# Kernel tuning notes

Hardware: AMD Instinct MI355X
Metric: run time of the kernel (lower is better)

The kernel has to match this reference:

```python
import jax, jax.numpy as jnp
import numpy as np

N_NODES = 100000
N_EDGES = 1200000
D = 64
GCN_LAYERS = 2
KEEP_PROB = 0.7


def setup_inputs() -> dict:
    key = jax.random.key(0)
    k1, k2, k3, k4, k5, k6, k7 = jax.random.split(key, 7)
    all_emb = jax.random.normal(k1, (N_NODES, D), dtype=jnp.float32)
    W = jax.random.normal(k2, (D, D), dtype=jnp.float32) * 0.05
    b = jax.random.normal(k3, (D,), dtype=jnp.float32) * 0.05
    # sparse adjacency values (e.g. normalized weights)
    vals = jax.random.uniform(k4, (N_EDGES,), dtype=jnp.float32)
    # per-layer dropout uniforms, mirrors torch.rand(len(values)) each layer
    drop_u = jax.random.uniform(k5, (GCN_LAYERS, N_EDGES), dtype=jnp.float32)
    rows = jax.random.randint(k6, (N_EDGES,), 0, N_NODES)
    cols = jax.random.randint(k7, (N_EDGES,), 0, N_NODES)
    return {"all_emb": all_emb, "W": W, "b": b, "vals": vals,
            "drop_u": drop_u, "rows": rows, "cols": cols}


def reference(all_emb, W, b, vals, drop_u, rows, cols):
    # emb[0] = fc(all_emb)
    acc = all_emb @ W.T + b  # [N, D]
    x = all_emb
    for layer in range(GCN_LAYERS):
        # edge dropout: keep iff (u + keep_prob) floors to 1, scale by 1/keep_prob
        keep = (drop_u[layer] + KEEP_PROB) >= 1.0
        v = jnp.where(keep, vals / KEEP_PROB, 0.0)  # [E]
        # SpMM: x <- A_dropped @ x via gather + segment-sum scatter
        msgs = v[:, None] * x[cols]  # [E, D]
        x = jax.ops.segment_sum(msgs, rows, num_segments=N_NODES)  # [N, D]
        acc = acc + x
    # mean over stacked (gcn_layers + 1) embeddings
    return acc / float(GCN_LAYERS + 1)
```

## Files before the change

kernel.cpp:

```cpp
#include <hip/hip_runtime.h>

#define N_NODES 100000
#define N_EDGES 1200000
#define D 64
#define KEEP_PROB 0.7f
#define INV_KEEP (1.0f / KEEP_PROB)
#define NBUCK 1564
#define MAXB 1024
#define PPART 256
#define CHUNK4 1172

#define ALOAD_I(p)   __hip_atomic_load((p), __ATOMIC_RELAXED, __HIP_MEMORY_SCOPE_AGENT)
#define ALOAD_U64(p) __hip_atomic_load((p), __ATOMIC_RELAXED, __HIP_MEMORY_SCOPE_AGENT)

__global__ __launch_bounds__(256) void zero_kernel(float4* __restrict__ p, int n4) {
    int i = blockIdx.x * 256 + threadIdx.x;
    if (i < n4) p[i] = make_float4(0.f, 0.f, 0.f, 0.f);
}
__global__ __launch_bounds__(256) void zero_ints_kernel(int* __restrict__ p, int n) {
    int i = blockIdx.x * 256 + threadIdx.x;
    if (i < n) p[i] = 0;
}

__global__ __launch_bounds__(256) void bucket_hist_kernel(const int4* __restrict__ rows4,
                                                          int* __restrict__ bcnt,
                                                          int* __restrict__ h) {
    __shared__ int hh[NBUCK];
    int p = blockIdx.x;
    int t = threadIdx.x;
    for (int i = t; i < NBUCK; i += 256) hh[i] = 0;
    __syncthreads();
    int i0 = p * CHUNK4;
    int i1 = i0 + CHUNK4;
    if (i1 > N_EDGES / 4) i1 = N_EDGES / 4;
    for (int i = i0 + t; i < i1; i += 256) {
        int4 r = rows4[i];
        atomicAdd(&hh[r.x >> 6], 1);
        atomicAdd(&hh[r.y >> 6], 1);
        atomicAdd(&hh[r.z >> 6], 1);
        atomicAdd(&hh[r.w >> 6], 1);
    }
    __syncthreads();
    int* hp = h + p * NBUCK;
    for (int i = t; i < NBUCK; i += 256) {
        int c = hh[i];
        hp[i] = c;
        if (c) atomicAdd(&bcnt[i << 4], c);
    }
}

__global__ __launch_bounds__(256) void bucket_scan_kernel(const int* __restrict__ bcnt,
                                                          int* __restrict__ bbase,
                                                          int* __restrict__ Pstart) {
    __shared__ int part[256];
    const int CH = 7;
    int t = threadIdx.x;
    int e[CH]; int s = 0;
    #pragma unroll
    for (int k = 0; k < CH; ++k) {
        int j = t * CH + k;
        e[k] = (j < NBUCK) ? ALOAD_I(&bcnt[j << 4]) : 0;
        s += e[k];
    }
    part[t] = s;
    __syncthreads();
    for (int d = 1; d < 256; d <<= 1) {
        int w = (t >= d) ? part[t - d] : 0;
        __syncthreads();
        part[t] += w;
        __syncthreads();
    }
    int run = part[t] - s;
    #pragma unroll
    for (int k = 0; k < CH; ++k) {
        int j = t * CH + k;
        if (j < NBUCK) { bbase[j] = run; run += e[k]; }
    }
    if (t == 255) bbase[NBUCK] = run;
    if (t == 0)   Pstart[N_NODES] = N_EDGES;
}

__global__ __launch_bounds__(256) void rebase_kernel(int* __restrict__ h,
                                                     const int* __restrict__ bbase) {
    int b = blockIdx.x * 256 + threadIdx.x;
    if (b >= NBUCK) return;
    int run = bbase[b];
    for (int p = 0; p < PPART; ++p) {
        int idx = p * NBUCK + b;
        int c = h[idx];
        h[idx] = run;
        run += c;
    }
}

__global__ __launch_bounds__(256) void partition_kernel(
    const int4*   __restrict__ rows4,
    const int4*   __restrict__ cols4,
    const float4* __restrict__ vals4,
    const float4* __restrict__ u04,
    const float4* __restrict__ u14,
    const int*    __restrict__ h,
    uint4*        __restrict__ edata) {
    __shared__ int cur[NBUCK];
    int p = blockIdx.x;
    int t = threadIdx.x;
    const int* hp = h + p * NBUCK;
    for (int i = t; i < NBUCK; i += 256) cur[i] = hp[i];
    __syncthreads();

    int i0 = p * CHUNK4;
    int i1 = i0 + CHUNK4;
    if (i1 > N_EDGES / 4) i1 = N_EDGES / 4;
    for (int i = i0 + t; i < i1; i += 256) {
        int4   r  = rows4[i];
        int4   c  = cols4[i];
        float4 v  = vals4[i];
        float4 u0 = u04[i];
        float4 u1 = u14[i];

        int p0 = atomicAdd(&cur[r.x >> 6], 1);
        int p1 = atomicAdd(&cur[r.y >> 6], 1);
        int p2 = atomicAdd(&cur[r.z >> 6], 1);
        int p3 = atomicAdd(&cur[r.w >> 6], 1);

        uint4 rec; float vv;
        vv = v.x * INV_KEEP;
        rec.x = (unsigned)c.x;
        rec.y = __float_as_uint((u0.x + KEEP_PROB >= 1.0f) ? vv : 0.f);
        rec.z = __float_as_uint((u1.x + KEEP_PROB >= 1.0f) ? vv : 0.f);
        rec.w = (unsigned)r.x;
        edata[p0] = rec;
        vv = v.y * INV_KEEP;
        rec.x = (unsigned)c.y;
        rec.y = __float_as_uint((u0.y + KEEP_PROB >= 1.0f) ? vv : 0.f);
        rec.z = __float_as_uint((u1.y + KEEP_PROB >= 1.0f) ? vv : 0.f);
        rec.w = (unsigned)r.y;
        edata[p1] = rec;
        vv = v.z * INV_KEEP;
        rec.x = (unsigned)c.z;
        rec.y = __float_as_uint((u0.z + KEEP_PROB >= 1.0f) ? vv : 0.f);
        rec.z = __float_as_uint((u1.z + KEEP_PROB >= 1.0f) ? vv : 0.f);
        rec.w = (unsigned)r.z;
        edata[p2] = rec;
        vv = v.w * INV_KEEP;
        rec.x = (unsigned)c.w;
        rec.y = __float_as_uint((u0.w + KEEP_PROB >= 1.0f) ? vv : 0.f);
        rec.z = __float_as_uint((u1.w + KEEP_PROB >= 1.0f) ? vv : 0.f);
        rec.w = (unsigned)r.w;
        edata[p3] = rec;
    }
}

__global__ __launch_bounds__(256) void finalize_kernel(
    uint4* __restrict__ edata,
    const int* __restrict__ bbase,
    int*   __restrict__ Pstart,
    uint4* __restrict__ scratch) {
    __shared__ uint4 recs[MAXB];
    __shared__ int cnt[64], cur[64], part[64];
    int b = blockIdx.x;
    int t = threadIdx.x;
    int base = bbase[b];
    int size = bbase[b + 1] - base;
    int row0 = b << 6;
    bool small = (size <= MAXB);

    const unsigned long long* src = (const unsigned long long*)(edata + base);
    if (small) {
        for (int i = t; i < size; i += 256) {
            unsigned long long lo = ALOAD_U64(src + 2 * i);
            unsigned long long hi = ALOAD_U64(src + 2 * i + 1);
            uint4 r;
            r.x = (unsigned)lo; r.y = (unsigned)(lo >> 32);
            r.z = (unsigned)hi; r.w = (unsigned)(hi >> 32);
            recs[i] = r;
        }
    } else {
        unsigned long long* dst = (unsigned long long*)(scratch + base);
        for (int i = t; i < 2 * size; i += 256) dst[i] = ALOAD_U64(src + i);
    }
    if (t < 64) cnt[t] = 0;
    __syncthreads();

    const uint4* gsrc = scratch + base;
    for (int i = t; i < size; i += 256) {
        unsigned rw = small ? recs[i].w : gsrc[i].w;
        atomicAdd(&cnt[rw & 63], 1);
    }
    __syncthreads();

    int v = (t < 64) ? cnt[t] : 0;
    if (t < 64) part[t] = v;
    __syncthreads();
    for (int d = 1; d < 64; d <<= 1) {
        int w = (t >= d && t < 64) ? part[t - d] : 0;
        __syncthreads();
        if (t < 64) part[t] += w;
        __syncthreads();
    }
    int R = N_NODES - row0; if (R > 64) R = 64;
    if (t < 64) {
        int pref = part[t] - v;
        cur[t] = pref;
        if (t < R) Pstart[row0 + t] = base + pref;
    }
    __syncthreads();

    for (int i = t; i < size; i += 256) {
        uint4 r = small ? recs[i] : gsrc[i];
        int lr = (int)(r.w & 63);
        int slot = atomicAdd(&cur[lr], 1);
        uint4 outrec;
        outrec.x = r.x; outrec.y = r.y;
        outrec.z = r.x; outrec.w = r.z;
        edata[base + slot] = outrec;
    }
}

__global__ __launch_bounds__(256) void spmm_gather_kernel(
    const float4* __restrict__ x_in,
    const unsigned long long* __restrict__ edata,
    const int*   __restrict__ Pstart,
    float4*      __restrict__ io,
    int layer) {
    int tid = blockIdx.x * 256 + threadIdx.x;
    int row = tid >> 4;
    int l16 = threadIdx.x & 15;
    if (row >= N_NODES) return;
    int start = ALOAD_I(&Pstart[row]);
    int end   = ALOAD_I(&Pstart[row + 1]);
    float4 acc = make_float4(0.f, 0.f, 0.f, 0.f);
    #pragma unroll 8
    for (int i = start; i < end; ++i) {
        unsigned long long rec = ALOAD_U64(&edata[2 * i + layer]);
        int   c = (int)(rec & 0xffffffffu);
        float v = __uint_as_float((unsigned)(rec >> 32));
        int  cc = (v != 0.f) ? c : 0;
        float4 x = x_in[(cc << 4) + l16];
        acc.x = fmaf(v, x.x, acc.x);
        acc.y = fmaf(v, x.y, acc.y);
        acc.z = fmaf(v, x.z, acc.z);
        acc.w = fmaf(v, x.w, acc.w);
    }
    int o = (row << 4) + l16;
    if (layer == 0) {
        io[o] = acc;
    } else {
        float4 p = io[o];
        p.x = (p.x + acc.x) * (1.0f / 3.0f);
        p.y = (p.y + acc.y) * (1.0f / 3.0f);
        p.z = (p.z + acc.z) * (1.0f / 3.0f);
        p.w = (p.w + acc.w) * (1.0f / 3.0f);
        io[o] = p;
    }
}

#define FMA4(A, E, WV) \
    A.x = fmaf(E, WV.x, A.x); A.y = fmaf(E, WV.y, A.y); \
    A.z = fmaf(E, WV.z, A.z); A.w = fmaf(E, WV.w, A.w);

__global__ __launch_bounds__(256, 4) void fc_add_kernel(
    const float* __restrict__ emb,
    const float* __restrict__ W,
    const float* __restrict__ b,
    const float* __restrict__ x1,
    float*       __restrict__ out) {
    __shared__ float Wt[D * 68];
    __shared__ float Es[64 * 68];

    int t = threadIdx.x;
    int n0 = blockIdx.x * 64;

    #pragma unroll
    for (int i = 0; i < 16; ++i) {
        int idx = i * 256 + t;
        Wt[(idx & 63) * 68 + (idx >> 6)] = W[idx];
    }
    #pragma unroll
    for (int i = 0; i < 4; ++i) {
        int idx4 = i * 256 + t;
        int n = idx4 >> 4;
        int k0 = (idx4 & 15) * 4;
        float4 v = make_float4(0.f, 0.f, 0.f, 0.f);
        if (n0 + n < N_NODES) v = *(const float4*)&emb[(n0 + n) * D + k0];
        *(float4*)&Es[n * 68 + k0] = v;
    }
    __syncthreads();

    int tj = t & 15;
    int tn = t >> 4;
    int j0 = tj * 4;

    float4 bb = *(const float4*)&b[j0];
    float4 acc[4];
    #pragma unroll
    for (int i = 0; i < 4; ++i) acc[i] = bb;

    const float* es = &Es[(tn * 4) * 68];
    #pragma unroll 4
    for (int kc = 0; kc < 16; ++kc) {
        int k = kc * 4;
        float4 w0 = *(const float4*)&Wt[(k + 0) * 68 + j0];
        float4 w1 = *(const float4*)&Wt[(k + 1) * 68 + j0];
        float4 w2 = *(const float4*)&Wt[(k + 2) * 68 + j0];
        float4 w3 = *(const float4*)&Wt[(k + 3) * 68 + j0];
        float4 e0 = *(const float4*)&es[0 * 68 + k];
        float4 e1 = *(const float4*)&es[1 * 68 + k];
        float4 e2 = *(const float4*)&es[2 * 68 + k];
        float4 e3 = *(const float4*)&es[3 * 68 + k];
        FMA4(acc[0], e0.x, w0); FMA4(acc[0], e0.y, w1);
        FMA4(acc[0], e0.z, w2); FMA4(acc[0], e0.w, w3);
        FMA4(acc[1], e1.x, w0); FMA4(acc[1], e1.y, w1);
        FMA4(acc[1], e1.z, w2); FMA4(acc[1], e1.w, w3);
        FMA4(acc[2], e2.x, w0); FMA4(acc[2], e2.y, w1);
        FMA4(acc[2], e2.z, w2); FMA4(acc[2], e2.w, w3);
        FMA4(acc[3], e3.x, w0); FMA4(acc[3], e3.y, w1);
        FMA4(acc[3], e3.z, w2); FMA4(acc[3], e3.w, w3);
    }

    #pragma unroll
    for (int i = 0; i < 4; ++i) {
        int n = n0 + tn * 4 + i;
        if (n < N_NODES) {
            float4 p = *(const float4*)&x1[n * D + j0];
            float4 a = acc[i];
            a.x += p.x; a.y += p.y; a.z += p.z; a.w += p.w;
            *(float4*)&out[n * D + j0] = a;
        }
    }
}

__global__ __launch_bounds__(256) void spmm_atomic_kernel(
    const float* __restrict__ x_in,
    const float* __restrict__ vals,
    const float* __restrict__ drop_u,
    const int*   __restrict__ rows,
    const int*   __restrict__ cols,
    float*       __restrict__ x_out) {
    int wave = (blockIdx.x * 256 + threadIdx.x) >> 6;
    int lane = threadIdx.x & 63;
    if (wave >= N_EDGES) return;
    float u = drop_u[wave];
    if (u + KEEP_PROB < 1.0f) return;
    float v = vals[wave] * INV_KEEP;
    atomicAdd(&x_out[rows[wave] * D + lane], v * x_in[cols[wave] * D + lane]);
}

__global__ __launch_bounds__(256) void scale_kernel(float4* __restrict__ p, int n4) {
    int i = blockIdx.x * 256 + threadIdx.x;
    if (i < n4) {
        float4 v = p[i];
        v.x *= (1.f/3.f); v.y *= (1.f/3.f); v.z *= (1.f/3.f); v.w *= (1.f/3.f);
        p[i] = v;
    }
}

extern "C" void kernel_launch(void* const* d_in, const int* in_sizes, int n_in,
                              void* d_out, int out_size, void* d_ws, size_t ws_size,
                              hipStream_t stream) {
    const float* all_emb = (const float*)d_in[0];
    const float* W       = (const float*)d_in[1];
    const float* b       = (const float*)d_in[2];
    const float* vals    = (const float*)d_in[3];
    const float* drop_u  = (const float*)d_in[4];
    const int*   rows    = (const int*)d_in[5];
    const int*   cols    = (const int*)d_in[6];

    float* out = (float*)d_out;

    char* ws = (char*)d_ws;
    float* x1     = (float*)(ws);
    int*   Pstart = (int*)  (ws + 25600000);
    uint4* edata  = (uint4*)(ws + 26000064);
    int*   bcnt   = (int*)  (ws + 45200064);
    int*   bbase  = (int*)  (ws + 45300160);
    int*   h      = (int*)  (ws + 19200000);
    const size_t WS_NEEDED = 45406528;

    const int n4 = N_NODES * D / 4;
    const int zb = (n4 + 255) / 256;
    const int gather_blocks = (N_NODES * 16 + 255) / 256;
    const int fc_blocks = (N_NODES + 63) / 64;

    if (ws_size >= WS_NEEDED) {
        zero_ints_kernel<<<(NBUCK * 16 + 255) / 256, 256, 0, stream>>>(bcnt, NBUCK * 16);
        bucket_hist_kernel<<<PPART, 256, 0, stream>>>((const int4*)rows, bcnt, h);
        bucket_scan_kernel<<<1, 256, 0, stream>>>(bcnt, bbase, Pstart);
        rebase_kernel<<<(NBUCK + 255) / 256, 256, 0, stream>>>(h, bbase);
        partition_kernel<<<PPART, 256, 0, stream>>>(
            (const int4*)rows, (const int4*)cols, (const float4*)vals,
            (const float4*)drop_u, (const float4*)(drop_u + N_EDGES),
            h, edata);
        finalize_kernel<<<NBUCK, 256, 0, stream>>>(edata, bbase, Pstart, (uint4*)x1);
        spmm_gather_kernel<<<gather_blocks, 256, 0, stream>>>(
            (const float4*)all_emb, (const unsigned long long*)edata, Pstart,
            (float4*)x1, 0);
        fc_add_kernel<<<fc_blocks, 256, 0, stream>>>(all_emb, W, b, x1, out);
        spmm_gather_kernel<<<gather_blocks, 256, 0, stream>>>(
            (const float4*)x1, (const unsigned long long*)edata, Pstart,
            (float4*)out, 1);
    } else {
        const int spmm_blocks = (N_EDGES + 3) / 4;
        zero_kernel<<<zb, 256, 0, stream>>>((float4*)x1, n4);
        spmm_atomic_kernel<<<spmm_blocks, 256, 0, stream>>>(all_emb, vals, drop_u,
                                                            rows, cols, x1);
        fc_add_kernel<<<fc_blocks, 256, 0, stream>>>(all_emb, W, b, x1, out);
        spmm_atomic_kernel<<<spmm_blocks, 256, 0, stream>>>(x1, vals,
                                                            drop_u + N_EDGES,
                                                            rows, cols, out);
        scale_kernel<<<zb, 256, 0, stream>>>((float4*)out, n4);
    }
}
```

Baseline: 280.4 us.

## Replace per-row CSR finalize with bucket-level SpMM using shared-memory atomics

Drops the finalize pass that sorted each 64-row bucket into per-row order and built row pointers. The row offset within the bucket is packed into the column word, and a new SpMM kernel processes one bucket per block, accumulating into a 64x64 shared-memory tile with atomics before writing out. This removes one kernel and a full read-write pass over the edge records. In exchange each SpMM edge costs four LDS float atomics, and the summation order becomes nondeterministic; a rotated column index is used to reduce bank conflicts.

After: 1.071 ms. 3.82x slower.

```diff
diff --git a/kernel.cpp b/kernel.cpp
--- a/kernel.cpp
+++ b/kernel.cpp
@@ -6,7 +6,6 @@
 #define KEEP_PROB 0.7f
 #define INV_KEEP (1.0f / KEEP_PROB)
 #define NBUCK 1564
-#define MAXB 1024
 #define PPART 256
 #define CHUNK4 1172
 
@@ -50,8 +49,7 @@
 }
 
 __global__ __launch_bounds__(256) void bucket_scan_kernel(const int* __restrict__ bcnt,
-                                                          int* __restrict__ bbase,
-                                                          int* __restrict__ Pstart) {
+                                                          int* __restrict__ bbase) {
     __shared__ int part[256];
     const int CH = 7;
     int t = threadIdx.x;
@@ -77,7 +75,6 @@
         if (j < NBUCK) { bbase[j] = run; run += e[k]; }
     }
     if (t == 255) bbase[NBUCK] = run;
-    if (t == 0)   Pstart[N_NODES] = N_EDGES;
 }
 
 __global__ __launch_bounds__(256) void rebase_kernel(int* __restrict__ h,
@@ -123,135 +120,105 @@
         int p2 = atomicAdd(&cur[r.z >> 6], 1);
         int p3 = atomicAdd(&cur[r.w >> 6], 1);
 
-        uint4 rec; float vv;
+        uint4 rec; float vv; unsigned cr;
         vv = v.x * INV_KEEP;
-        rec.x = (unsigned)c.x;
+        cr = (unsigned)c.x | (((unsigned)r.x & 63u) << 17);
+        rec.x = cr;
         rec.y = __float_as_uint((u0.x + KEEP_PROB >= 1.0f) ? vv : 0.f);
-        rec.z = __float_as_uint((u1.x + KEEP_PROB >= 1.0f) ? vv : 0.f);
-        rec.w = (unsigned)r.x;
+        rec.z = cr;
+        rec.w = __float_as_uint((u1.x + KEEP_PROB >= 1.0f) ? vv : 0.f);
         edata[p0] = rec;
         vv = v.y * INV_KEEP;
-        rec.x = (unsigned)c.y;
+        cr = (unsigned)c.y | (((unsigned)r.y & 63u) << 17);
+        rec.x = cr;
         rec.y = __float_as_uint((u0.y + KEEP_PROB >= 1.0f) ? vv : 0.f);
-        rec.z = __float_as_uint((u1.y + KEEP_PROB >= 1.0f) ? vv : 0.f);
-        rec.w = (unsigned)r.y;
+        rec.z = cr;
+        rec.w = __float_as_uint((u1.y + KEEP_PROB >= 1.0f) ? vv : 0.f);
         edata[p1] = rec;
         vv = v.z * INV_KEEP;
-        rec.x = (unsigned)c.z;
+        cr = (unsigned)c.z | (((unsigned)r.z & 63u) << 17);
+        rec.x = cr;
         rec.y = __float_as_uint((u0.z + KEEP_PROB >= 1.0f) ? vv : 0.f);
-        rec.z = __float_as_uint((u1.z + KEEP_PROB >= 1.0f) ? vv : 0.f);
-        rec.w = (unsigned)r.z;
+        rec.z = cr;
+        rec.w = __float_as_uint((u1.z + KEEP_PROB >= 1.0f) ? vv : 0.f);
         edata[p2] = rec;
         vv = v.w * INV_KEEP;
-        rec.x = (unsigned)c.w;
+        cr = (unsigned)c.w | (((unsigned)r.w & 63u) << 17);
+        rec.x = cr;
         rec.y = __float_as_uint((u0.w + KEEP_PROB >= 1.0f) ? vv : 0.f);
-        rec.z = __float_as_uint((u1.w + KEEP_PROB >= 1.0f) ? vv : 0.f);
-        rec.w = (unsigned)r.w;
+        rec.z = cr;
+        rec.w = __float_as_uint((u1.w + KEEP_PROB >= 1.0f) ? vv : 0.f);
         edata[p3] = rec;
     }
 }
 
-__global__ __launch_bounds__(256) void finalize_kernel(
-    uint4* __restrict__ edata,
-    const int* __restrict__ bbase,
-    int*   __restrict__ Pstart,
-    uint4* __restrict__ scratch) {
-    __shared__ uint4 recs[MAXB];
-    __shared__ int cnt[64], cur[64], part[64];
+__global__ __launch_bounds__(256) void spmm_bucket_kernel(
+    const float4* __restrict__ x_in,
+    const unsigned long long* __restrict__ edata,
+    const int*   __restrict__ bbase,
+    float4*      __restrict__ io,
+    int layer) {
+    __shared__ float accs[64 * 64];
     int b = blockIdx.x;
     int t = threadIdx.x;
     int base = bbase[b];
     int size = bbase[b + 1] - base;
     int row0 = b << 6;
-    bool small = (size <= MAXB);
-
-    const unsigned long long* src = (const unsigned long long*)(edata + base);
-    if (small) {
-        for (int i = t; i < size; i += 256) {
-            unsigned long long lo = ALOAD_U64(src + 2 * i);
-            unsigned long long hi = ALOAD_U64(src + 2 * i + 1);
-            uint4 r;
-            r.x = (unsigned)lo; r.y = (unsigned)(lo >> 32);
-            r.z = (unsigned)hi; r.w = (unsigned)(hi >> 32);
-            recs[i] = r;
+
+    #pragma unroll
+    for (int i = 0; i < 4; ++i)
+        *(float4*)&accs[(i * 256 + t) * 4] = make_float4(0.f, 0.f, 0.f, 0.f);
+    __syncthreads();
+
+    int g   = t >> 4;
+    int l16 = t & 15;
+    int e0 = base + ((size * g) >> 4);
+    int e1 = base + ((size * (g + 1)) >> 4);
+    int j0 = l16 << 2;
+
+    #pragma unroll 8
+    for (int e = e0; e < e1; ++e) {
+        unsigned long long rec = ALOAD_U64(&edata[2 * e + layer]);
+        unsigned lo = (unsigned)rec;
+        float v = __uint_as_float((unsigned)(rec >> 32));
+        int c  = (int)(lo & 0x1ffffu);
+        int lr = (int)(lo >> 17);
+        int cc = (v != 0.f) ? c : 0;
+        float4 x = x_in[(cc << 4) + l16];
+        float* arow = &accs[lr << 6];
+        atomicAdd(&arow[(j0 + 0 + lr) & 63], v * x.x);
+        atomicAdd(&arow[(j0 + 1 + lr) & 63], v * x.y);
+        atomicAdd(&arow[(j0 + 2 + lr) & 63], v * x.z);
+        atomicAdd(&arow[(j0 + 3 + lr) & 63], v * x.w);
+    }
+    __syncthreads();
+
+    #pragma unroll
+    for (int i = 0; i < 4; ++i) {
+        int idx = i * 256 + t;
+        int lr = idx >> 4;
+        int gg = idx & 15;
+        int row = row0 + lr;
+        if (row < N_NODES) {
+            const float* arow = &accs[lr << 6];
+            int s0 = (gg * 4 + lr) & 63;
+            float4 sv;
+            sv.x = arow[s0];
+            sv.y = arow[(s0 + 1) & 63];
+            sv.z = arow[(s0 + 2) & 63];
+            sv.w = arow[(s0 + 3) & 63];
+            int o = (row << 4) + gg;
+            if (layer == 0) {
+                io[o] = sv;
+            } else {
+                float4 p = io[o];
+                p.x = (p.x + sv.x) * (1.0f / 3.0f);
+                p.y = (p.y + sv.y) * (1.0f / 3.0f);
+                p.z = (p.z + sv.z) * (1.0f / 3.0f);
+                p.w = (p.w + sv.w) * (1.0f / 3.0f);
+                io[o] = p;
+            }
         }
-    } else {
-        unsigned long long* dst = (unsigned long long*)(scratch + base);
-        for (int i = t; i < 2 * size; i += 256) dst[i] = ALOAD_U64(src + i);
-    }
-    if (t < 64) cnt[t] = 0;
-    __syncthreads();
-
-    const uint4* gsrc = scratch + base;
-    for (int i = t; i < size; i += 256) {
-        unsigned rw = small ? recs[i].w : gsrc[i].w;
-        atomicAdd(&cnt[rw & 63], 1);
-    }
-    __syncthreads();
-
-    int v = (t < 64) ? cnt[t] : 0;
-    if (t < 64) part[t] = v;
-    __syncthreads();
-    for (int d = 1; d < 64; d <<= 1) {
-        int w = (t >= d && t < 64) ? part[t - d] : 0;
-        __syncthreads();
-        if (t < 64) part[t] += w;
-        __syncthreads();
-    }
-    int R = N_NODES - row0; if (R > 64) R = 64;
-    if (t < 64) {
-        int pref = part[t] - v;
-        cur[t] = pref;
-        if (t < R) Pstart[row0 + t] = base + pref;
-    }
-    __syncthreads();
-
-    for (int i = t; i < size; i += 256) {
-        uint4 r = small ? recs[i] : gsrc[i];
-        int lr = (int)(r.w & 63);
-        int slot = atomicAdd(&cur[lr], 1);
-        uint4 outrec;
-        outrec.x = r.x; outrec.y = r.y;
-        outrec.z = r.x; outrec.w = r.z;
-        edata[base + slot] = outrec;
-    }
-}
-
-__global__ __launch_bounds__(256) void spmm_gather_kernel(
-    const float4* __restrict__ x_in,
-    const unsigned long long* __restrict__ edata,
-    const int*   __restrict__ Pstart,
-    float4*      __restrict__ io,
-    int layer) {
-    int tid = blockIdx.x * 256 + threadIdx.x;
-    int row = tid >> 4;
-    int l16 = threadIdx.x & 15;
-    if (row >= N_NODES) return;
-    int start = ALOAD_I(&Pstart[row]);
-    int end   = ALOAD_I(&Pstart[row + 1]);
-    float4 acc = make_float4(0.f, 0.f, 0.f, 0.f);
-    #pragma unroll 8
-    for (int i = start; i < end; ++i) {
-        unsigned long long rec = ALOAD_U64(&edata[2 * i + layer]);
-        int   c = (int)(rec & 0xffffffffu);
-        float v = __uint_as_float((unsigned)(rec >> 32));
-        int  cc = (v != 0.f) ? c : 0;
-        float4 x = x_in[(cc << 4) + l16];
-        acc.x = fmaf(v, x.x, acc.x);
-        acc.y = fmaf(v, x.y, acc.y);
-        acc.z = fmaf(v, x.z, acc.z);
-        acc.w = fmaf(v, x.w, acc.w);
-    }
-    int o = (row << 4) + l16;
-    if (layer == 0) {
-        io[o] = acc;
-    } else {
-        float4 p = io[o];
-        p.x = (p.x + acc.x) * (1.0f / 3.0f);
-        p.y = (p.y + acc.y) * (1.0f / 3.0f);
-        p.z = (p.z + acc.z) * (1.0f / 3.0f);
-        p.w = (p.w + acc.w) * (1.0f / 3.0f);
-        io[o] = p;
     }
 }
 
@@ -370,7 +337,6 @@
 
     char* ws = (char*)d_ws;
     float* x1     = (float*)(ws);
-    int*   Pstart = (int*)  (ws + 25600000);
     uint4* edata  = (uint4*)(ws + 26000064);
     int*   bcnt   = (int*)  (ws + 45200064);
     int*   bbase  = (int*)  (ws + 45300160);
@@ -379,25 +345,23 @@
 
     const int n4 = N_NODES * D / 4;
     const int zb = (n4 + 255) / 256;
-    const int gather_blocks = (N_NODES * 16 + 255) / 256;
     const int fc_blocks = (N_NODES + 63) / 64;
 
     if (ws_size >= WS_NEEDED) {
         zero_ints_kernel<<<(NBUCK * 16 + 255) / 256, 256, 0, stream>>>(bcnt, NBUCK * 16);
         bucket_hist_kernel<<<PPART, 256, 0, stream>>>((const int4*)rows, bcnt, h);
-        bucket_scan_kernel<<<1, 256, 0, stream>>>(bcnt, bbase, Pstart);
+        bucket_scan_kernel<<<1, 256, 0, stream>>>(bcnt, bbase);
         rebase_kernel<<<(NBUCK + 255) / 256, 256, 0, stream>>>(h, bbase);
         partition_kernel<<<PPART, 256, 0, stream>>>(
             (const int4*)rows, (const int4*)cols, (const float4*)vals,
             (const float4*)drop_u, (const float4*)(drop_u + N_EDGES),
             h, edata);
-        finalize_kernel<<<NBUCK, 256, 0, stream>>>(edata, bbase, Pstart, (uint4*)x1);
-        spmm_gather_kernel<<<gather_blocks, 256, 0, stream>>>(
-            (const float4*)all_emb, (const unsigned long long*)edata, Pstart,
+        spmm_bucket_kernel<<<NBUCK, 256, 0, stream>>>(
+            (const float4*)all_emb, (const unsigned long long*)edata, bbase,
             (float4*)x1, 0);
         fc_add_kernel<<<fc_blocks, 256, 0, stream>>>(all_emb, W, b, x1, out);
-        spmm_gather_kernel<<<gather_blocks, 256, 0, stream>>>(
-            (const float4*)x1, (const unsigned long long*)edata, Pstart,
+        spmm_bucket_kernel<<<NBUCK, 256, 0, stream>>>(
+            (const float4*)x1, (const unsigned long long*)edata, bbase,
             (float4*)out, 1);
     } else {
         const int spmm_blocks = (N_EDGES + 3) / 4;
```

## Replace row-per-group SpMM with per-bucket edge-balanced gather and shared reduction

Applied to the files above, without the earlier changes.

The SpMM no longer walks per-row CSR offsets. Each block handles one 64-row bucket, and its 16 thread groups each take an equal slice of the bucket's edges. Local row ids are packed into the high bits of the column field, so row boundaries are found inline; partial rows at slice edges are merged through shared memory. This drops the Pstart array and its writes, and is meant to balance load across rows with skewed degree. The cost is fewer, larger blocks (1564), shared-memory accumulation with extra syncs, and per-edge branch overhead.

Result: no change. 281.3 us (+0.3%).

```diff
diff --git a/kernel.cpp b/kernel.cpp
--- a/kernel.cpp
+++ b/kernel.cpp
@@ -50,8 +50,7 @@
 }
 
 __global__ __launch_bounds__(256) void bucket_scan_kernel(const int* __restrict__ bcnt,
-                                                          int* __restrict__ bbase,
-                                                          int* __restrict__ Pstart) {
+                                                          int* __restrict__ bbase) {
     __shared__ int part[256];
     const int CH = 7;
     int t = threadIdx.x;
@@ -77,7 +76,6 @@
         if (j < NBUCK) { bbase[j] = run; run += e[k]; }
     }
     if (t == 255) bbase[NBUCK] = run;
-    if (t == 0)   Pstart[N_NODES] = N_EDGES;
 }
 
 __global__ __launch_bounds__(256) void rebase_kernel(int* __restrict__ h,
@@ -154,7 +152,6 @@
 __global__ __launch_bounds__(256) void finalize_kernel(
     uint4* __restrict__ edata,
     const int* __restrict__ bbase,
-    int*   __restrict__ Pstart,
     uint4* __restrict__ scratch) {
     __shared__ uint4 recs[MAXB];
     __shared__ int cnt[64], cur[64], part[64];
@@ -162,7 +159,6 @@
     int t = threadIdx.x;
     int base = bbase[b];
     int size = bbase[b + 1] - base;
-    int row0 = b << 6;
     bool small = (size <= MAXB);
 
     const unsigned long long* src = (const unsigned long long*)(edata + base);
@@ -198,60 +194,127 @@
         if (t < 64) part[t] += w;
         __syncthreads();
     }
-    int R = N_NODES - row0; if (R > 64) R = 64;
-    if (t < 64) {
-        int pref = part[t] - v;
-        cur[t] = pref;
-        if (t < R) Pstart[row0 + t] = base + pref;
-    }
+    if (t < 64) cur[t] = part[t] - v;
     __syncthreads();
 
     for (int i = t; i < size; i += 256) {
         uint4 r = small ? recs[i] : gsrc[i];
-        int lr = (int)(r.w & 63);
+        unsigned lr = r.w & 63u;
         int slot = atomicAdd(&cur[lr], 1);
+        unsigned cr = r.x | (lr << 17);
         uint4 outrec;
-        outrec.x = r.x; outrec.y = r.y;
-        outrec.z = r.x; outrec.w = r.z;
+        outrec.x = cr; outrec.y = r.y;
+        outrec.z = cr; outrec.w = r.z;
         edata[base + slot] = outrec;
     }
 }
 
-__global__ __launch_bounds__(256) void spmm_gather_kernel(
+__global__ __launch_bounds__(256) void spmm_flat_kernel(
     const float4* __restrict__ x_in,
     const unsigned long long* __restrict__ edata,
-    const int*   __restrict__ Pstart,
+    const int*   __restrict__ bbase,
     float4*      __restrict__ io,
     int layer) {
-    int tid = blockIdx.x * 256 + threadIdx.x;
-    int row = tid >> 4;
-    int l16 = threadIdx.x & 15;
-    if (row >= N_NODES) return;
-    int start = ALOAD_I(&Pstart[row]);
-    int end   = ALOAD_I(&Pstart[row + 1]);
+    __shared__ float accs[64 * 64];
+    __shared__ float partb[16][64];
+    __shared__ int   prow[16];
+    int b = blockIdx.x;
+    int t = threadIdx.x;
+    int base = bbase[b];
+    int size = bbase[b + 1] - base;
+    int row0 = b << 6;
+
+    #pragma unroll
+    for (int i = 0; i < 4; ++i)
+        *(float4*)&accs[(i * 256 + t) * 4] = make_float4(0.f, 0.f, 0.f, 0.f);
+    if (t < 16) prow[t] = -1;
+    __syncthreads();
+
+    int g   = t >> 4;
+    int l16 = t & 15;
+    int e0 = base + ((size * g) >> 4);
+    int e1 = base + ((size * (g + 1)) >> 4);
+    int j0 = l16 << 2;
+
+    bool partial = false;
+    if (e0 < e1 && e0 > base) {
+        unsigned plo = (unsigned)ALOAD_U64(&edata[2 * (e0 - 1) + layer]);
+        unsigned flo = (unsigned)ALOAD_U64(&edata[2 * e0 + layer]);
+        partial = ((plo >> 17) == (flo >> 17));
+    }
+
     float4 acc = make_float4(0.f, 0.f, 0.f, 0.f);
-    #pragma unroll 8
-    for (int i = start; i < end; ++i) {
-        unsigned long long rec = ALOAD_U64(&edata[2 * i + layer]);
-        int   c = (int)(rec & 0xffffffffu);
+    int cur = -1;
+    bool first = true;
+    for (int e = e0; e < e1; ++e) {
+        unsigned long long rec = ALOAD_U64(&edata[2 * e + layer]);
+        unsigned lo = (unsigned)rec;
         float v = __uint_as_float((unsigned)(rec >> 32));
-        int  cc = (v != 0.f) ? c : 0;
+        int lr = (int)(lo >> 17);
+        if (lr != cur) {
+            if (cur >= 0) {
+                if (first && partial) {
+                    *(float4*)&partb[g][j0] = acc;
+                    if (l16 == 0) prow[g] = cur;
+                } else {
+                    *(float4*)&accs[(cur << 6) + j0] = acc;
+                }
+                first = false;
+            }
+            acc = make_float4(0.f, 0.f, 0.f, 0.f);
+            cur = lr;
+        }
+        int c  = (int)(lo & 0x1ffffu);
+        int cc = (v != 0.f) ? c : 0;
         float4 x = x_in[(cc << 4) + l16];
         acc.x = fmaf(v, x.x, acc.x);
         acc.y = fmaf(v, x.y, acc.y);
         acc.z = fmaf(v, x.z, acc.z);
         acc.w = fmaf(v, x.w, acc.w);
     }
-    int o = (row << 4) + l16;
-    if (layer == 0) {
-        io[o] = acc;
-    } else {
-        float4 p = io[o];
-        p.x = (p.x + acc.x) * (1.0f / 3.0f);
-        p.y = (p.y + acc.y) * (1.0f / 3.0f);
-        p.z = (p.z + acc.z) * (1.0f / 3.0f);
-        p.w = (p.w + acc.w) * (1.0f / 3.0f);
-        io[o] = p;
+    if (cur >= 0) {
+        if (first && partial) {
+            *(float4*)&partb[g][j0] = acc;
+            if (l16 == 0) prow[g] = cur;
+        } else {
+            *(float4*)&accs[(cur << 6) + j0] = acc;
+        }
+    }
+    __syncthreads();
+
+    if (t < 16) {
+        int jj = t << 2;
+        for (int gg = 1; gg < 16; ++gg) {
+            int pr = prow[gg];
+            if (pr >= 0) {
+                float* a = &accs[(pr << 6) + jj];
+                const float* p = &partb[gg][jj];
+                a[0] += p[0]; a[1] += p[1]; a[2] += p[2]; a[3] += p[3];
+            }
+        }
+    }
+    __syncthreads();
+
+    #pragma unroll
+    for (int i = 0; i < 4; ++i) {
+        int idx = i * 256 + t;
+        int lr = idx >> 4;
+        int gg = idx & 15;
+        int row = row0 + lr;
+        if (row < N_NODES) {
+            float4 sv = *(const float4*)&accs[(lr << 6) + (gg << 2)];
+            int o = (row << 4) + gg;
+            if (layer == 0) {
+                io[o] = sv;
+            } else {
+                float4 p = io[o];
+                p.x = (p.x + sv.x) * (1.0f / 3.0f);
+                p.y = (p.y + sv.y) * (1.0f / 3.0f);
+                p.z = (p.z + sv.z) * (1.0f / 3.0f);
+                p.w = (p.w + sv.w) * (1.0f / 3.0f);
+                io[o] = p;
+            }
+        }
     }
 }
 
@@ -370,7 +433,6 @@
 
     char* ws = (char*)d_ws;
     float* x1     = (float*)(ws);
-    int*   Pstart = (int*)  (ws + 25600000);
     uint4* edata  = (uint4*)(ws + 26000064);
     int*   bcnt   = (int*)  (ws + 45200064);
     int*   bbase  = (int*)  (ws + 45300160);
@@ -379,25 +441,24 @@
 
     const int n4 = N_NODES * D / 4;
     const int zb = (n4 + 255) / 256;
-    const int gather_blocks = (N_NODES * 16 + 255) / 256;
     const int fc_blocks = (N_NODES + 63) / 64;
 
     if (ws_size >= WS_NEEDED) {
         zero_ints_kernel<<<(NBUCK * 16 + 255) / 256, 256, 0, stream>>>(bcnt, NBUCK * 16);
         bucket_hist_kernel<<<PPART, 256, 0, stream>>>((const int4*)rows, bcnt, h);
-        bucket_scan_kernel<<<1, 256, 0, stream>>>(bcnt, bbase, Pstart);
+        bucket_scan_kernel<<<1, 256, 0, stream>>>(bcnt, bbase);
         rebase_kernel<<<(NBUCK + 255) / 256, 256, 0, stream>>>(h, bbase);
         partition_kernel<<<PPART, 256, 0, stream>>>(
             (const int4*)rows, (const int4*)cols, (const float4*)vals,
             (const float4*)drop_u, (const float4*)(drop_u + N_EDGES),
             h, edata);
-        finalize_kernel<<<NBUCK, 256, 0, stream>>>(edata, bbase, Pstart, (uint4*)x1);
-        spmm_gather_kernel<<<gather_blocks, 256, 0, stream>>>(
-            (const float4*)all_emb, (const unsigned long long*)edata, Pstart,
+        finalize_kernel<<<NBUCK, 256, 0, stream>>>(edata, bbase, (uint4*)x1);
+        spmm_flat_kernel<<<NBUCK, 256, 0, stream>>>(
+            (const float4*)all_emb, (const unsigned long long*)edata, bbase,
             (float4*)x1, 0);
         fc_add_kernel<<<fc_blocks, 256, 0, stream>>>(all_emb, W, b, x1, out);
-        spmm_gather_kernel<<<gather_blocks, 256, 0, stream>>>(
-            (const float4*)x1, (const unsigned long long*)edata, Pstart,
+        spmm_flat_kernel<<<NBUCK, 256, 0, stream>>>(
+            (const float4*)x1, (const unsigned long long*)edata, bbase,
             (float4*)out, 1);
     } else {
         const int spmm_blocks = (N_EDGES + 3) / 4;
```
